# Kernel tuning notes

Measured on AMD Instinct MI355X. Metric: run time of the kernel, lower is better.

The kernel has to match this reference:

```python
import jax, jax.numpy as jnp
import numpy as np

NUM_CLASS = 4096
HIDDEN = 512
N_GROUPS = 64  # per branch (co and cl)
BATCH = 64


def _make_group_of(rng, n_groups, num_class):
    # Ragged partition of [0, num_class) into n_groups contiguous segments,
    # mirroring len_co_list_index offsets of the original module.
    cuts = np.sort(rng.choice(np.arange(1, num_class), size=n_groups - 1, replace=False))
    sizes = np.diff(np.concatenate([[0], cuts, [num_class]]))
    return np.repeat(np.arange(n_groups), sizes)  # [num_class] -> group id per class slot


def setup_inputs() -> dict:
    key = jax.random.key(0)
    k_x, k_cow, k_clw, k_cob, k_clb = jax.random.split(key, 5)
    rng = np.random.default_rng(0)
    stdv = 1.0 / np.sqrt(HIDDEN)  # matches reset_parameters uniform(-stdv, stdv)

    x = jax.random.normal(k_x, (BATCH, 2 * N_GROUPS, HIDDEN), dtype=jnp.float32)
    co_W = jax.random.uniform(k_cow, (1, NUM_CLASS, HIDDEN), jnp.float32, -stdv, stdv)
    cl_W = jax.random.uniform(k_clw, (1, NUM_CLASS, HIDDEN), jnp.float32, -stdv, stdv)
    co_b = jax.random.uniform(k_cob, (1, NUM_CLASS), jnp.float32, -stdv, stdv)
    cl_b = jax.random.uniform(k_clb, (1, NUM_CLASS), jnp.float32, -stdv, stdv)

    co_group_of = jnp.asarray(_make_group_of(rng, N_GROUPS, NUM_CLASS), jnp.int32)
    cl_group_of = jnp.asarray(_make_group_of(rng, N_GROUPS, NUM_CLASS), jnp.int32)
    # co_index / cl_index are class-id permutations applied after concat
    co_index = jnp.asarray(rng.permutation(NUM_CLASS), jnp.int32)
    cl_index = jnp.asarray(rng.permutation(NUM_CLASS), jnp.int32)

    return {
        "x": x,
        "co_W": co_W, "cl_W": cl_W,
        "co_b": co_b, "cl_b": cl_b,
        "co_group_of": co_group_of, "cl_group_of": cl_group_of,
        "co_index": co_index, "cl_index": cl_index,
        "group_len": N_GROUPS,
    }


def reference(x, co_W, cl_W, co_b, cl_b, co_group_of, cl_group_of, co_index, cl_index, group_len):
    # x: [B, 2*G, H]; first G group-features feed the co branch, rest the cl branch.
    co_x = x[:, :group_len, :]   # [B, G, H]
    cl_x = x[:, group_len:, :]   # [B, G, H]

    # Fused ragged group-wise broadcast-multiply + reduce:
    # out[b, c] = dot(W[0, c], x[b, group_of[c]]) + b[0, c]
    co_out = jnp.einsum("bch,ch->bc", co_x[:, co_group_of, :], co_W[0]) + co_b  # [B, C]
    cl_out = jnp.einsum("bch,ch->bc", cl_x[:, cl_group_of, :], cl_W[0]) + cl_b  # [B, C]

    # Final index_select gather over classes
    return co_out[:, co_index], cl_out[:, cl_index]
```

## Files before the change

kernel.cpp:

```cpp
#include <hip/hip_runtime.h>
#include <hip/hip_bf16.h>
#include <string.h>

#define NUM_CLASS 4096
#define HIDDEN    512
#define NGROUPS   64
#define BATCH     64

#define WS_INV   10240
#define TMP_OFF_F 16384
#define TMP_H_STRIDE (4096*64)
#define TMP_S_STRIDE (2*4096*64)

typedef __attribute__((ext_vector_type(8))) short short8;
typedef __attribute__((ext_vector_type(4))) float f32x4;

__device__ __forceinline__ unsigned int pack2bf(float a, float b) {
    __hip_bfloat16 ha = __float2bfloat16(a), hb = __float2bfloat16(b);
    unsigned short ua, ub;
    memcpy(&ua, &ha, 2); memcpy(&ub, &hb, 2);
    return (unsigned int)ua | ((unsigned int)ub << 16);
}

__global__ __launch_bounds__(1024) void prep_inv_kernel(
    const int* __restrict__ co_idx, const int* __restrict__ cl_idx,
    int* __restrict__ ws)
{
    int tid = threadIdx.x;
    for (int v = tid; v < 2 * NUM_CLASS; v += 1024) {
        int h = v >> 12, c = v & (NUM_CLASS - 1);
        const int* idx = h ? cl_idx : co_idx;
        ws[WS_INV + h * NUM_CLASS + idx[c]] = c;
    }
}

template<int KS, bool SCATTER>
__global__ __launch_bounds__(256, 4) void gwl_stage1(
    const float* __restrict__ x,
    const float* __restrict__ co_W, const float* __restrict__ cl_W,
    const float* __restrict__ co_b, const float* __restrict__ cl_b,
    const int* __restrict__ co_gof, const int* __restrict__ cl_gof,
    int* __restrict__ ws, float* __restrict__ out)
{
    const int NCH = 8 / KS;
    const int nblk = 128 * KS;
    const int chunk = nblk >> 3;
    int bid = blockIdx.x;
    int swz = (bid & 7) * chunk + (bid >> 3);
    int cid = swz & 63;
    int hk  = swz >> 6;
    int h   = hk & 1;
    int kh  = hk >> 1;
    int c0  = cid * 64;

    const float* Wp  = h ? cl_W : co_W;
    const int*   gof = h ? cl_gof : co_gof;

    __shared__ __align__(16) unsigned short Xs[64][72];
    __shared__ __align__(16) unsigned short Wls[64][72];
    __shared__ float ftile[64][65];
    __shared__ int s_seg_lo[65];
    __shared__ int s_seg_g[64];
    __shared__ int s_nseg;

    int tid = threadIdx.x;
    int l = tid & 63, w = tid >> 6;

    if (tid < 64) {
        int gi = gof[c0 + tid];
        int prev = (tid == 0) ? -1 : gof[c0 + tid - 1];
        bool is_start = (gi != prev);
        unsigned long long m = __ballot(is_start);
        int segidx = (int)__popcll(m & ((1ull << tid) - 1ull));
        if (is_start) { s_seg_lo[segidx] = tid; s_seg_g[segidx] = gi; }
        if (tid == 0) {
            int ns = (int)__popcll(m);
            s_nseg = ns;
            s_seg_lo[ns] = 64;
        }
    }

    int rowq[4], kvq[4];
    #pragma unroll
    for (int q = 0; q < 4; ++q) {
        int v = q * 256 + tid;
        rowq[q] = v >> 4;
        kvq[q]  = v & 15;
    }

    float4 rxA[4], rwA[4], rxB[4], rwB[4];
    f32x4 acc[4];
    #pragma unroll
    for (int i = 0; i < 4; ++i) acc[i] = (f32x4)(0.0f);

    const int kbase = kh * (HIDDEN / KS);

#define LOADC(S, RX, RW, NEEDW) do {                                                \
    int si_ = (S) / NCH, t_ = (S) % NCH;                                            \
    int k0_ = kbase + t_ * 64;                                                      \
    int xr_ = h * 64 + s_seg_g[si_];                                                \
    _Pragma("unroll")                                                               \
    for (int q = 0; q < 4; ++q) {                                                   \
        RX[q] = *(const float4*)(x + rowq[q] * 65536 + xr_ * 512 + k0_ + kvq[q]*4); \
        if (NEEDW)                                                                  \
            RW[q] = *(const float4*)(Wp + (c0 + rowq[q]) * 512 + k0_ + kvq[q] * 4); \
    } } while (0)

#define STOREC(RX, RW, NEEDW) do {                                                  \
    _Pragma("unroll")                                                               \
    for (int q = 0; q < 4; ++q) {                                                   \
        unsigned int x0 = pack2bf(RX[q].x, RX[q].y);                                \
        unsigned int x1 = pack2bf(RX[q].z, RX[q].w);                                \
        *(uint2*)&Xs[rowq[q]][kvq[q] * 4] = make_uint2(x0, x1);                     \
        if (NEEDW) {                                                                \
            unsigned int w0 = pack2bf(RW[q].x, RW[q].y);                            \
            unsigned int w1 = pack2bf(RW[q].z, RW[q].w);                            \
            *(uint2*)&Wls[rowq[q]][kvq[q] * 4] = make_uint2(w0, w1);                \
        }                                                                           \
    } } while (0)

#define COMPUTEC() do {                                                             \
    _Pragma("unroll")                                                               \
    for (int kq = 0; kq < 2; ++kq) {                                                \
        int koff = kq * 32 + (l >> 4) * 8;                                          \
        short8 bfrag = *(const short8*)&Wls[w * 16 + (l & 15)][koff];               \
        _Pragma("unroll")                                                           \
        for (int i = 0; i < 4; ++i) {                                               \
            short8 afrag = *(const short8*)&Xs[16 * i + (l & 15)][koff];            \
            acc[i] = __builtin_amdgcn_mfma_f32_16x16x32_bf16(afrag, bfrag, acc[i],  \
                                                             0, 0, 0);              \
        }                                                                           \
    } } while (0)

    __syncthreads();
    int nseg = s_nseg;
    int nsteps = nseg * NCH;
    int slotw = w * 16 + (l & 15);

    LOADC(0, rxA, rwA, true);
    STOREC(rxA, rwA, true);
    __syncthreads();

    #pragma unroll 1
    for (int s = 0; s < nsteps; ++s) {
        bool nxt = (s + 1 < nsteps);
        const bool needW = (NCH > 1);
        if (nxt) {
            if (s & 1) LOADC(s + 1, rxA, rwA, needW);
            else       LOADC(s + 1, rxB, rwB, needW);
        }
        COMPUTEC();
        if ((s % NCH) == NCH - 1) {
            int si = s / NCH;
            int lo = s_seg_lo[si], hi = s_seg_lo[si + 1];
            if (slotw >= lo && slotw < hi) {
                #pragma unroll
                for (int i = 0; i < 4; ++i)
                    #pragma unroll
                    for (int r = 0; r < 4; ++r)
                        ftile[slotw][16 * i + (l >> 4) * 4 + r] = acc[i][r];
            }
            #pragma unroll
            for (int i = 0; i < 4; ++i) acc[i] = (f32x4)(0.0f);
        }
        __syncthreads();
        if (nxt) {
            if (s & 1) STOREC(rxA, rwA, needW);
            else       STOREC(rxB, rwB, needW);
            __syncthreads();
        }
    }

    if (!SCATTER) {
        float* tmph = (float*)ws + TMP_OFF_F + (size_t)(kh * 2 + h) * TMP_H_STRIDE;
        #pragma unroll
        for (int p = 0; p < 4; ++p) {
            int f = p * 256 + tid;
            int slot = f >> 4, b4 = (f & 15) * 4;
            *(float4*)&tmph[(size_t)(c0 + slot) * 64 + b4] =
                *(const float4*)&ftile[slot][b4];
        }
    } else {
        const float* bias = h ? cl_b : co_b;
        const int*   inv  = ws + WS_INV + h * NUM_CLASS;
        float* outh = out + (size_t)h * BATCH * NUM_CLASS;
        #pragma unroll
        for (int p = 0; p < 4; ++p) {
            int f = p * 256 + tid;
            int slot = f >> 4, b4 = (f & 15) * 4;
            int c = c0 + slot;
            int oc = inv[c];
            float bb = bias[c];
            #pragma unroll
            for (int e = 0; e < 4; ++e)
                outh[(b4 + e) * 4096 + oc] = ftile[slot][b4 + e] + bb;
        }
    }
#undef LOADC
#undef STOREC
#undef COMPUTEC
}

template<int KS>
__global__ __launch_bounds__(256) void gwl_permute(
    const int* __restrict__ ws,
    const float* __restrict__ co_b, const float* __restrict__ cl_b,
    const int* __restrict__ co_idx, const int* __restrict__ cl_idx,
    float* __restrict__ out)
{
    int jc = blockIdx.x;
    int h  = blockIdx.y;
    const float* bias = h ? cl_b : co_b;
    const int*   idx  = h ? cl_idx : co_idx;
    const float* tmph = (const float*)ws + TMP_OFF_F + (size_t)h * TMP_H_STRIDE;

    __shared__ float tile[64][65];
    int tid = threadIdx.x;
    int lane = tid & 63, w = tid >> 6;

    #pragma unroll
    for (int u = 0; u < 16; ++u) {
        int jj = u * 4 + w;
        int j  = jc * 64 + jj;
        int c  = idx[j];
        float v = bias[c];
        #pragma unroll
        for (int s = 0; s < KS; ++s)
            v += tmph[(size_t)s * TMP_S_STRIDE + (size_t)c * 64 + lane];
        tile[lane][jj] = v;
    }
    __syncthreads();

    #pragma unroll
    for (int p = 0; p < 4; ++p) {
        int f = p * 256 + tid;
        int b = f >> 4, j4 = (f & 15) * 4;
        *(float4*)&out[((size_t)h * 64 + b) * 4096 + jc * 64 + j4] =
            *(const float4*)&tile[b][j4];
    }
}

extern "C" void kernel_launch(void* const* d_in, const int* in_sizes, int n_in,
                              void* d_out, int out_size, void* d_ws, size_t ws_size,
                              hipStream_t stream)
{
    (void)in_sizes; (void)n_in; (void)out_size;
    const float* x      = (const float*)d_in[0];
    const float* co_W   = (const float*)d_in[1];
    const float* cl_W   = (const float*)d_in[2];
    const float* co_b   = (const float*)d_in[3];
    const float* cl_b   = (const float*)d_in[4];
    const int*   co_gof = (const int*)d_in[5];
    const int*   cl_gof = (const int*)d_in[6];
    const int*   co_idx = (const int*)d_in[7];
    const int*   cl_idx = (const int*)d_in[8];
    int*   ws  = (int*)d_ws;
    float* out = (float*)d_out;

    const size_t base  = (size_t)TMP_OFF_F * 4;
    const size_t slice = (size_t)TMP_S_STRIDE * 4;

    if (ws_size >= base + 8 * slice) {
        hipLaunchKernelGGL((gwl_stage1<8, false>), dim3(1024), dim3(256), 0, stream,
                           x, co_W, cl_W, co_b, cl_b, co_gof, cl_gof, ws, out);
        hipLaunchKernelGGL((gwl_permute<8>), dim3(64, 2), dim3(256), 0, stream,
                           ws, co_b, cl_b, co_idx, cl_idx, out);
    } else if (ws_size >= base + 4 * slice) {
        hipLaunchKernelGGL((gwl_stage1<4, false>), dim3(512), dim3(256), 0, stream,
                           x, co_W, cl_W, co_b, cl_b, co_gof, cl_gof, ws, out);
        hipLaunchKernelGGL((gwl_permute<4>), dim3(64, 2), dim3(256), 0, stream,
                           ws, co_b, cl_b, co_idx, cl_idx, out);
    } else if (ws_size >= base + 2 * slice) {
        hipLaunchKernelGGL((gwl_stage1<2, false>), dim3(256), dim3(256), 0, stream,
                           x, co_W, cl_W, co_b, cl_b, co_gof, cl_gof, ws, out);
        hipLaunchKernelGGL((gwl_permute<2>), dim3(64, 2), dim3(256), 0, stream,
                           ws, co_b, cl_b, co_idx, cl_idx, out);
    } else if (ws_size >= base + 1 * slice) {
        hipLaunchKernelGGL((gwl_stage1<1, false>), dim3(128), dim3(256), 0, stream,
                           x, co_W, cl_W, co_b, cl_b, co_gof, cl_gof, ws, out);
        hipLaunchKernelGGL((gwl_permute<1>), dim3(64, 2), dim3(256), 0, stream,
                           ws, co_b, cl_b, co_idx, cl_idx, out);
    } else {
        hipLaunchKernelGGL(prep_inv_kernel, dim3(1), dim3(1024), 0, stream,
                           co_idx, cl_idx, ws);
        hipLaunchKernelGGL((gwl_stage1<1, true>), dim3(128), dim3(256), 0, stream,
                           x, co_W, cl_W, co_b, cl_b, co_gof, cl_gof, ws, out);
    }
}
```

Baseline: 23.32 us.

## Replace LDS-staged stage1 with direct-to-register MFMA GEMM and smaller permute tiles

The split-K stage1 kernel is replaced by a version that loads W and x fragments straight from global memory into registers, converts them to bf16 and feeds the MFMA without staging through shared memory or block barriers. Partial results go straight to the temp buffer. The default split changes from 8 to 4 K-slices, which cuts the permute kernel's reduction reads, and the permute kernel now uses 32-column tiles to launch more blocks. The cost is uncoalesced per-lane global loads, more registers (occupancy hint lowered to 2), and less parallelism in the GEMM stage.

After: 45.82 us. +96.5%, slower.

```diff
diff --git a/kernel.cpp b/kernel.cpp
--- a/kernel.cpp
+++ b/kernel.cpp
@@ -22,6 +22,13 @@
     return (unsigned int)ua | ((unsigned int)ub << 16);
 }
 
+__device__ __forceinline__ short8 cvt8(float4 a, float4 b) {
+    union { short8 s; unsigned int u[4]; } r;
+    r.u[0] = pack2bf(a.x, a.y); r.u[1] = pack2bf(a.z, a.w);
+    r.u[2] = pack2bf(b.x, b.y); r.u[3] = pack2bf(b.z, b.w);
+    return r.s;
+}
+
 __global__ __launch_bounds__(1024) void prep_inv_kernel(
     const int* __restrict__ co_idx, const int* __restrict__ cl_idx,
     int* __restrict__ ws)
@@ -34,38 +41,30 @@
     }
 }
 
-template<int KS, bool SCATTER>
-__global__ __launch_bounds__(256, 4) void gwl_stage1(
+template<int KS>
+__global__ __launch_bounds__(256, 2) void gwl_gemm_direct(
     const float* __restrict__ x,
     const float* __restrict__ co_W, const float* __restrict__ cl_W,
-    const float* __restrict__ co_b, const float* __restrict__ cl_b,
     const int* __restrict__ co_gof, const int* __restrict__ cl_gof,
-    int* __restrict__ ws, float* __restrict__ out)
-{
-    const int NCH = 8 / KS;
+    float* __restrict__ tmp)
+{
+    const int KQ = (HIDDEN / KS) / 32;
     const int nblk = 128 * KS;
     const int chunk = nblk >> 3;
     int bid = blockIdx.x;
     int swz = (bid & 7) * chunk + (bid >> 3);
-    int cid = swz & 63;
-    int hk  = swz >> 6;
-    int h   = hk & 1;
-    int kh  = hk >> 1;
-    int c0  = cid * 64;
+    int cid = swz & 63, hk = swz >> 6;
+    int h = hk & 1, kh = hk >> 1;
+    int c0 = cid * 64;
 
     const float* Wp  = h ? cl_W : co_W;
     const int*   gof = h ? cl_gof : co_gof;
 
-    __shared__ __align__(16) unsigned short Xs[64][72];
-    __shared__ __align__(16) unsigned short Wls[64][72];
-    __shared__ float ftile[64][65];
     __shared__ int s_seg_lo[65];
     __shared__ int s_seg_g[64];
     __shared__ int s_nseg;
 
     int tid = threadIdx.x;
-    int l = tid & 63, w = tid >> 6;
-
     if (tid < 64) {
         int gi = gof[c0 + tid];
         int prev = (tid == 0) ? -1 : gof[c0 + tid - 1];
@@ -79,6 +78,135 @@
             s_seg_lo[ns] = 64;
         }
     }
+    __syncthreads();
+
+    int l = tid & 63, w = tid >> 6;
+    int kbase = kh * (HIDDEN / KS);
+    int kcol  = kbase + (l >> 4) * 8;
+    int crow  = c0 + w * 16 + (l & 15);
+    int brow  = l & 15;
+
+    short8 bfrag[KQ];
+    #pragma unroll
+    for (int kq = 0; kq < KQ; ++kq) {
+        const float* wp = Wp + (size_t)crow * 512 + kcol + kq * 32;
+        bfrag[kq] = cvt8(*(const float4*)wp, *(const float4*)(wp + 4));
+    }
+
+    float* tmph = tmp + (size_t)(kh * 2 + h) * TMP_H_STRIDE;
+    int nseg  = s_nseg;
+    int slotw = w * 16 + (l & 15);
+
+    #pragma unroll 1
+    for (int si = 0; si < nseg; ++si) {
+        int xr = h * 64 + s_seg_g[si];
+        const float* xp = x + (size_t)xr * 512 + kcol;
+        f32x4 acc[4];
+        #pragma unroll
+        for (int i = 0; i < 4; ++i) acc[i] = (f32x4)(0.0f);
+
+        #pragma unroll
+        for (int kq = 0; kq < KQ; ++kq) {
+            #pragma unroll
+            for (int i = 0; i < 4; ++i) {
+                const float* ap = xp + (size_t)(16 * i + brow) * 65536 + kq * 32;
+                short8 af = cvt8(*(const float4*)ap, *(const float4*)(ap + 4));
+                acc[i] = __builtin_amdgcn_mfma_f32_16x16x32_bf16(
+                             af, bfrag[kq], acc[i], 0, 0, 0);
+            }
+        }
+
+        int lo = s_seg_lo[si], hi = s_seg_lo[si + 1];
+        if (slotw >= lo && slotw < hi) {
+            float* tr = tmph + (size_t)crow * 64 + (l >> 4) * 4;
+            #pragma unroll
+            for (int i = 0; i < 4; ++i)
+                *(f32x4*)(tr + 16 * i) = acc[i];
+        }
+    }
+}
+
+template<int KS>
+__global__ __launch_bounds__(256) void gwl_permute32(
+    const float* __restrict__ tmp,
+    const float* __restrict__ co_b, const float* __restrict__ cl_b,
+    const int* __restrict__ co_idx, const int* __restrict__ cl_idx,
+    float* __restrict__ out)
+{
+    int jc = blockIdx.x;
+    int h  = blockIdx.y;
+    const float* bias = h ? cl_b : co_b;
+    const int*   idx  = h ? cl_idx : co_idx;
+    const float* tmph = tmp + (size_t)h * TMP_H_STRIDE;
+
+    __shared__ float tile[64][33];
+    int tid = threadIdx.x;
+    int lane = tid & 63, w = tid >> 6;
+
+    #pragma unroll
+    for (int u = 0; u < 8; ++u) {
+        int jj = u * 4 + w;
+        int j  = jc * 32 + jj;
+        int c  = idx[j];
+        float v = bias[c];
+        #pragma unroll
+        for (int s = 0; s < KS; ++s)
+            v += tmph[(size_t)s * TMP_S_STRIDE + (size_t)c * 64 + lane];
+        tile[lane][jj] = v;
+    }
+    __syncthreads();
+
+    #pragma unroll
+    for (int p = 0; p < 2; ++p) {
+        int f = p * 256 + tid;
+        int b = f >> 3, j4 = (f & 7) * 4;
+        *(float4*)&out[((size_t)h * 64 + b) * 4096 + jc * 32 + j4] =
+            *(const float4*)&tile[b][j4];
+    }
+}
+
+__global__ __launch_bounds__(256, 4) void gwl_stage1_scatter(
+    const float* __restrict__ x,
+    const float* __restrict__ co_W, const float* __restrict__ cl_W,
+    const float* __restrict__ co_b, const float* __restrict__ cl_b,
+    const int* __restrict__ co_gof, const int* __restrict__ cl_gof,
+    int* __restrict__ ws, float* __restrict__ out)
+{
+    const int KS = 1, NCH = 8;
+    const int nblk = 128;
+    const int chunk = nblk >> 3;
+    int bid = blockIdx.x;
+    int swz = (bid & 7) * chunk + (bid >> 3);
+    int cid = swz & 63;
+    int h   = swz >> 6;
+    int c0  = cid * 64;
+
+    const float* Wp  = h ? cl_W : co_W;
+    const int*   gof = h ? cl_gof : co_gof;
+
+    __shared__ __align__(16) unsigned short Xs[64][72];
+    __shared__ __align__(16) unsigned short Wls[64][72];
+    __shared__ float ftile[64][65];
+    __shared__ int s_seg_lo[65];
+    __shared__ int s_seg_g[64];
+    __shared__ int s_nseg;
+
+    int tid = threadIdx.x;
+    int l = tid & 63, w = tid >> 6;
+
+    if (tid < 64) {
+        int gi = gof[c0 + tid];
+        int prev = (tid == 0) ? -1 : gof[c0 + tid - 1];
+        bool is_start = (gi != prev);
+        unsigned long long m = __ballot(is_start);
+        int segidx = (int)__popcll(m & ((1ull << tid) - 1ull));
+        if (is_start) { s_seg_lo[segidx] = tid; s_seg_g[segidx] = gi; }
+        if (tid == 0) {
+            int ns = (int)__popcll(m);
+            s_nseg = ns;
+            s_seg_lo[ns] = 64;
+        }
+    }
 
     int rowq[4], kvq[4];
     #pragma unroll
@@ -93,11 +221,9 @@
     #pragma unroll
     for (int i = 0; i < 4; ++i) acc[i] = (f32x4)(0.0f);
 
-    const int kbase = kh * (HIDDEN / KS);
-
 #define LOADC(S, RX, RW, NEEDW) do {                                                \
     int si_ = (S) / NCH, t_ = (S) % NCH;                                            \
-    int k0_ = kbase + t_ * 64;                                                      \
+    int k0_ = t_ * 64;                                                              \
     int xr_ = h * 64 + s_seg_g[si_];                                                \
     _Pragma("unroll")                                                               \
     for (int q = 0; q < 4; ++q) {                                                   \
@@ -144,10 +270,9 @@
     #pragma unroll 1
     for (int s = 0; s < nsteps; ++s) {
         bool nxt = (s + 1 < nsteps);
-        const bool needW = (NCH > 1);
         if (nxt) {
-            if (s & 1) LOADC(s + 1, rxA, rwA, needW);
-            else       LOADC(s + 1, rxB, rwB, needW);
+            if (s & 1) LOADC(s + 1, rxA, rwA, true);
+            else       LOADC(s + 1, rxB, rwB, true);
         }
         COMPUTEC();
         if ((s % NCH) == NCH - 1) {
@@ -165,79 +290,29 @@
         }
         __syncthreads();
         if (nxt) {
-            if (s & 1) STOREC(rxA, rwA, needW);
-            else       STOREC(rxB, rwB, needW);
+            if (s & 1) STOREC(rxA, rwA, true);
+            else       STOREC(rxB, rwB, true);
             __syncthreads();
         }
     }
 
-    if (!SCATTER) {
-        float* tmph = (float*)ws + TMP_OFF_F + (size_t)(kh * 2 + h) * TMP_H_STRIDE;
+    const float* bias = h ? cl_b : co_b;
+    const int*   inv  = ws + WS_INV + h * NUM_CLASS;
+    float* outh = out + (size_t)h * BATCH * NUM_CLASS;
+    #pragma unroll
+    for (int p = 0; p < 4; ++p) {
+        int f = p * 256 + tid;
+        int slot = f >> 4, b4 = (f & 15) * 4;
+        int c = c0 + slot;
+        int oc = inv[c];
+        float bb = bias[c];
         #pragma unroll
-        for (int p = 0; p < 4; ++p) {
-            int f = p * 256 + tid;
-            int slot = f >> 4, b4 = (f & 15) * 4;
-            *(float4*)&tmph[(size_t)(c0 + slot) * 64 + b4] =
-                *(const float4*)&ftile[slot][b4];
-        }
-    } else {
-        const float* bias = h ? cl_b : co_b;
-        const int*   inv  = ws + WS_INV + h * NUM_CLASS;
-        float* outh = out + (size_t)h * BATCH * NUM_CLASS;
-        #pragma unroll
-        for (int p = 0; p < 4; ++p) {
-            int f = p * 256 + tid;
-            int slot = f >> 4, b4 = (f & 15) * 4;
-            int c = c0 + slot;
-            int oc = inv[c];
-            float bb = bias[c];
-            #pragma unroll
-            for (int e = 0; e < 4; ++e)
-                outh[(b4 + e) * 4096 + oc] = ftile[slot][b4 + e] + bb;
-        }
+        for (int e = 0; e < 4; ++e)
+            outh[(b4 + e) * 4096 + oc] = ftile[slot][b4 + e] + bb;
     }
 #undef LOADC
 #undef STOREC
 #undef COMPUTEC
-}
-
-template<int KS>
-__global__ __launch_bounds__(256) void gwl_permute(
-    const int* __restrict__ ws,
-    const float* __restrict__ co_b, const float* __restrict__ cl_b,
-    const int* __restrict__ co_idx, const int* __restrict__ cl_idx,
-    float* __restrict__ out)
-{
-    int jc = blockIdx.x;
-    int h  = blockIdx.y;
-    const float* bias = h ? cl_b : co_b;
-    const int*   idx  = h ? cl_idx : co_idx;
-    const float* tmph = (const float*)ws + TMP_OFF_F + (size_t)h * TMP_H_STRIDE;
-
-    __shared__ float tile[64][65];
-    int tid = threadIdx.x;
-    int lane = tid & 63, w = tid >> 6;
-
-    #pragma unroll
-    for (int u = 0; u < 16; ++u) {
-        int jj = u * 4 + w;
-        int j  = jc * 64 + jj;
-        int c  = idx[j];
-        float v = bias[c];
-        #pragma unroll
-        for (int s = 0; s < KS; ++s)
-            v += tmph[(size_t)s * TMP_S_STRIDE + (size_t)c * 64 + lane];
-        tile[lane][jj] = v;
-    }
-    __syncthreads();
-
-    #pragma unroll
-    for (int p = 0; p < 4; ++p) {
-        int f = p * 256 + tid;
-        int b = f >> 4, j4 = (f & 15) * 4;
-        *(float4*)&out[((size_t)h * 64 + b) * 4096 + jc * 64 + j4] =
-            *(const float4*)&tile[b][j4];
-    }
 }
 
 extern "C" void kernel_launch(void* const* d_in, const int* in_sizes, int n_in,
@@ -255,35 +330,31 @@
     const int*   co_idx = (const int*)d_in[7];
     const int*   cl_idx = (const int*)d_in[8];
     int*   ws  = (int*)d_ws;
+    float* tmp = (float*)d_ws + TMP_OFF_F;
     float* out = (float*)d_out;
 
     const size_t base  = (size_t)TMP_OFF_F * 4;
     const size_t slice = (size_t)TMP_S_STRIDE * 4;
 
-    if (ws_size >= base + 8 * slice) {
-        hipLaunchKernelGGL((gwl_stage1<8, false>), dim3(1024), dim3(256), 0, stream,
-                           x, co_W, cl_W, co_b, cl_b, co_gof, cl_gof, ws, out);
-        hipLaunchKernelGGL((gwl_permute<8>), dim3(64, 2), dim3(256), 0, stream,
-                           ws, co_b, cl_b, co_idx, cl_idx, out);
-    } else if (ws_size >= base + 4 * slice) {
-        hipLaunchKernelGGL((gwl_stage1<4, false>), dim3(512), dim3(256), 0, stream,
-                           x, co_W, cl_W, co_b, cl_b, co_gof, cl_gof, ws, out);
-        hipLaunchKernelGGL((gwl_permute<4>), dim3(64, 2), dim3(256), 0, stream,
-                           ws, co_b, cl_b, co_idx, cl_idx, out);
+    if (ws_size >= base + 4 * slice) {
+        hipLaunchKernelGGL((gwl_gemm_direct<4>), dim3(512), dim3(256), 0, stream,
+                           x, co_W, cl_W, co_gof, cl_gof, tmp);
+        hipLaunchKernelGGL((gwl_permute32<4>), dim3(128, 2), dim3(256), 0, stream,
+                           tmp, co_b, cl_b, co_idx, cl_idx, out);
     } else if (ws_size >= base + 2 * slice) {
-        hipLaunchKernelGGL((gwl_stage1<2, false>), dim3(256), dim3(256), 0, stream,
-                           x, co_W, cl_W, co_b, cl_b, co_gof, cl_gof, ws, out);
-        hipLaunchKernelGGL((gwl_permute<2>), dim3(64, 2), dim3(256), 0, stream,
-                           ws, co_b, cl_b, co_idx, cl_idx, out);
+        hipLaunchKernelGGL((gwl_gemm_direct<2>), dim3(256), dim3(256), 0, stream,
+                           x, co_W, cl_W, co_gof, cl_gof, tmp);
+        hipLaunchKernelGGL((gwl_permute32<2>), dim3(128, 2), dim3(256), 0, stream,
+                           tmp, co_b, cl_b, co_idx, cl_idx, out);
     } else if (ws_size >= base + 1 * slice) {
-        hipLaunchKernelGGL((gwl_stage1<1, false>), dim3(128), dim3(256), 0, stream,
-                           x, co_W, cl_W, co_b, cl_b, co_gof, cl_gof, ws, out);
-        hipLaunchKernelGGL((gwl_permute<1>), dim3(64, 2), dim3(256), 0, stream,
-                           ws, co_b, cl_b, co_idx, cl_idx, out);
+        hipLaunchKernelGGL((gwl_gemm_direct<1>), dim3(128), dim3(256), 0, stream,
+                           x, co_W, cl_W, co_gof, cl_gof, tmp);
+        hipLaunchKernelGGL((gwl_permute32<1>), dim3(128, 2), dim3(256), 0, stream,
+                           tmp, co_b, cl_b, co_idx, cl_idx, out);
     } else {
         hipLaunchKernelGGL(prep_inv_kernel, dim3(1), dim3(1024), 0, stream,
                            co_idx, cl_idx, ws);
-        hipLaunchKernelGGL((gwl_stage1<1, true>), dim3(128), dim3(256), 0, stream,
+        hipLaunchKernelGGL(gwl_stage1_scatter, dim3(128), dim3(256), 0, stream,
                            x, co_W, cl_W, co_b, cl_b, co_gof, cl_gof, ws, out);
     }
 }
```
